# Kernel optimization log

Hardware: AMD Instinct MI355X
Metric: run time of the kernel (lower is better)

The kernel has to match this reference:

```python
import jax, jax.numpy as jnp
import numpy as np

N_NODES = 50000
N_EDGES = 400000
D_IN = 2048
D_OUT = 512


def setup_inputs() -> dict:
    key = jax.random.key(0)
    k1, k2, k3 = jax.random.split(key, 3)
    x = jax.random.normal(k1, (N_NODES, D_IN), dtype=jnp.float32)
    edge_index = jax.random.randint(k2, (2, N_EDGES), 0, N_NODES, dtype=jnp.int64)
    # Glorot init like PyG GCNConv
    scale = jnp.sqrt(6.0 / (D_IN + D_OUT)).astype(jnp.float32)
    weight = jax.random.uniform(k3, (D_IN, D_OUT), dtype=jnp.float32, minval=-scale, maxval=scale)
    bias = jnp.zeros((D_OUT,), dtype=jnp.float32)
    return {"x": x, "edge_index": edge_index, "weight": weight, "bias": bias}


def reference(x, edge_index, weight, bias):
    N = x.shape[0]
    # GCNConv(normalize=True): add self-loops, symmetric deg^-1/2 normalization
    loops = jnp.arange(N, dtype=edge_index.dtype)
    src = jnp.concatenate([edge_index[0], loops])  # message sources (x_j)
    dst = jnp.concatenate([edge_index[1], loops])  # aggregation targets
    ones = jnp.ones(dst.shape[0], dtype=x.dtype)
    deg = jax.ops.segment_sum(ones, dst, num_segments=N)  # [N]
    deg_inv_sqrt = jnp.where(deg > 0, jax.lax.rsqrt(deg), 0.0)
    norm = deg_inv_sqrt[src] * deg_inv_sqrt[dst]  # [E+N]
    h = x @ weight  # [N, d_out] linear transform before propagation
    msgs = norm[:, None] * h[src]  # [E+N, d_out]
    out = jax.ops.segment_sum(msgs, dst, num_segments=N) + bias  # [N, d_out]
    return jax.nn.log_softmax(out, axis=1)
```

## Files before the change

kernel.cpp:

```cpp
#include <hip/hip_runtime.h>
#include <stdint.h>

#define D_IN   2048
#define D_OUT  512

typedef __bf16 bf16;
typedef bf16     bf16x8 __attribute__((ext_vector_type(8)));
typedef float    f32x4  __attribute__((ext_vector_type(4)));
typedef uint32_t u32x4  __attribute__((ext_vector_type(4)));

#define GLP(p)  (const __attribute__((address_space(1))) void*)(p)
#define LDSP(p) (__attribute__((address_space(3))) void*)(p)

__global__ void k_count(const int* __restrict__ dstv, int* __restrict__ cnt, int E) {
    int e = blockIdx.x * blockDim.x + threadIdx.x;
    if (e < E) atomicAdd(&cnt[dstv[e]], 1);
}

__global__ __launch_bounds__(1024) void k_scan1(const int* __restrict__ cnt,
                                                int* __restrict__ offs,
                                                int* __restrict__ bsum,
                                                float* __restrict__ dis,
                                                int* __restrict__ cur, int n) {
    __shared__ int wsum[16], wbase[16];
    const int tid = threadIdx.x, lane = tid & 63, wv = tid >> 6;
    int i = blockIdx.x * 1024 + tid;
    int v = (i < n) ? cnt[i] : 0;
    int x = v;
    #pragma unroll
    for (int d = 1; d < 64; d <<= 1) {
        int y = __shfl_up(x, d);
        if (lane >= d) x += y;
    }
    if (lane == 63) wsum[wv] = x;
    __syncthreads();
    if (tid < 16) {
        int s = 0;
        for (int j = 0; j < tid; ++j) s += wsum[j];
        wbase[tid] = s;
    }
    __syncthreads();
    if (i < n) {
        offs[i] = wbase[wv] + x - v;
        dis[i]  = rsqrtf((float)(v + 1));
        cur[i]  = 0;
    }
    if (tid == 0) bsum[blockIdx.x] = wbase[15] + wsum[15];
}

__global__ void k_scan2(int* __restrict__ bsum, int nb) {
    int t = threadIdx.x;
    if (nb <= 64) {
        int v = (t < nb) ? bsum[t] : 0;
        int x = v;
        #pragma unroll
        for (int d = 1; d < 64; d <<= 1) {
            int y = __shfl_up(x, d);
            if (t >= d) x += y;
        }
        if (t < nb) bsum[t] = x - v;
    } else if (t == 0) {
        int run = 0;
        for (int j = 0; j < nb; ++j) { int v = bsum[j]; bsum[j] = run; run += v; }
    }
}

__global__ void k_fill(const int* __restrict__ srcv, const int* __restrict__ dstv,
                       const int* __restrict__ offs, const int* __restrict__ bsum,
                       const float* __restrict__ dis, int* __restrict__ cur,
                       int* __restrict__ csr, float* __restrict__ nrm, int E) {
    int e = blockIdx.x * blockDim.x + threadIdx.x;
    if (e < E) {
        int d = dstv[e];
        int s = srcv[e];
        int p = offs[d] + bsum[d >> 10] + atomicAdd(&cur[d], 1);
        csr[p] = s;
        nrm[p] = dis[s];
    }
}

__global__ void k_wt(const float* __restrict__ W, uint16_t* __restrict__ wt) {
    __shared__ float t[32][33];
    int kb = blockIdx.x * 32, nb = blockIdx.y * 32;
    int tx = threadIdx.x, ty = threadIdx.y;
    #pragma unroll
    for (int i = 0; i < 32; i += 8)
        t[ty + i][tx] = W[(size_t)(kb + ty + i) * D_OUT + nb + tx];
    __syncthreads();
    bf16* o = (bf16*)wt;
    #pragma unroll
    for (int i = 0; i < 32; i += 8)
        o[(size_t)(nb + ty + i) * D_IN + kb + tx] = (bf16)t[tx][ty + i];
}

__global__ __launch_bounds__(256, 3) void k_gemm(const float* __restrict__ X,
                                                 const uint16_t* __restrict__ WT,
                                                 uint16_t* __restrict__ H, int M) {
    __shared__ uint16_t lsA[128 * 64];
    __shared__ uint16_t lsB[2][128 * 64];
    const int nwg = gridDim.x;
    const int b = blockIdx.x;
    const int q = nwg >> 3, r = nwg & 7;
    const int xcd = b & 7, lo = b >> 3;
    const int g = (xcd < r) ? (xcd * (q + 1) + lo) : (r * (q + 1) + (xcd - r) * q + lo);
    const int m0 = (g >> 2) * 128;
    const int n0 = (g & 3) * 128;
    const int tid = threadIdx.x;
    const int w = tid >> 6, lane = tid & 63;
    const int wr = w >> 1, wc = w & 1;
    const int lr = lane & 15, lk = lane >> 4;
    const int NT = D_IN / 64;

    f32x4 acc[4][4];
    #pragma unroll
    for (int m = 0; m < 4; m++)
        #pragma unroll
        for (int n = 0; n < 4; n++) acc[m][n] = (f32x4)(0.0f);

    const float* aSrc[4];
    int aDst[4];
    const uint16_t* bSrc[4];
    #pragma unroll
    for (int j = 0; j < 4; j++) {
        int uidx = (w * 4 + j) * 64 + lane;
        int row = uidx >> 3, u = uidx & 7;
        int lrow = row;
        if (m0 + row >= M) lrow = (M - 1) - m0;
        aSrc[j] = X + (size_t)(m0 + lrow) * D_IN + u * 8;
        aDst[j] = row * 64 + (u ^ (row & 7)) * 8;
        bSrc[j] = WT + (size_t)(n0 + row) * D_IN + (u ^ (row & 7)) * 8;
    }

    f32x4 ar[8];

    auto loadA = [&](int t) {
        t &= (NT - 1);
        #pragma unroll
        for (int j = 0; j < 4; j++) {
            ar[2 * j]     = *(const f32x4*)(aSrc[j] + t * 64);
            ar[2 * j + 1] = *(const f32x4*)(aSrc[j] + t * 64 + 4);
        }
    };
    auto writeA = [&]() {
        #pragma unroll
        for (int j = 0; j < 4; j++) {
            f32x4 a0 = ar[2 * j], a1 = ar[2 * j + 1];
            bf16x8 tv;
            tv[0] = (bf16)a0[0]; tv[1] = (bf16)a0[1]; tv[2] = (bf16)a0[2]; tv[3] = (bf16)a0[3];
            tv[4] = (bf16)a1[0]; tv[5] = (bf16)a1[1]; tv[6] = (bf16)a1[2]; tv[7] = (bf16)a1[3];
            *(bf16x8*)(&lsA[aDst[j]]) = tv;
        }
    };
    auto stageB = [&](int t, int buf) {
        t &= (NT - 1);
        #pragma unroll
        for (int j = 0; j < 4; j++)
            __builtin_amdgcn_global_load_lds(GLP(bSrc[j] + t * 64),
                                             LDSP(&lsB[buf][(w * 4 + j) * 512]), 16, 0, 0);
    };
    auto compute = [&](int buf) {
        #pragma unroll
        for (int kk = 0; kk < 2; kk++) {
            bf16x8 aF[4], bF[4];
            #pragma unroll
            for (int m = 0; m < 4; m++) {
                int row = wr * 64 + m * 16 + lr;
                aF[m] = *(const bf16x8*)(&lsA[row * 64 + (((kk * 4 + lk) ^ (row & 7)) * 8)]);
            }
            #pragma unroll
            for (int n = 0; n < 4; n++) {
                int row = wc * 64 + n * 16 + lr;
                bF[n] = *(const bf16x8*)(&lsB[buf][row * 64 + (((kk * 4 + lk) ^ (row & 7)) * 8)]);
            }
            #pragma unroll
            for (int m = 0; m < 4; m++)
                #pragma unroll
                for (int n = 0; n < 4; n++)
                    acc[m][n] = __builtin_amdgcn_mfma_f32_16x16x32_bf16(aF[m], bF[n], acc[m][n], 0, 0, 0);
        }
    };

    loadA(0);
    stageB(0, 0);
    stageB(1, 1);
    asm volatile("s_waitcnt vmcnt(8)" ::: "memory");
    writeA();
    asm volatile("s_waitcnt vmcnt(4)" ::: "memory");
    asm volatile("s_waitcnt lgkmcnt(0)" ::: "memory");
    __builtin_amdgcn_s_barrier();

    #pragma unroll 1
    for (int t = 0; t < NT; t += 2) {
        loadA(t + 1);
        compute(0);
        __builtin_amdgcn_s_barrier();
        stageB(t + 2, 0);
        asm volatile("s_waitcnt vmcnt(4)" ::: "memory");
        writeA();
        asm volatile("s_waitcnt lgkmcnt(0)" ::: "memory");
        __builtin_amdgcn_s_barrier();
        loadA(t + 2);
        compute(1);
        __builtin_amdgcn_s_barrier();
        stageB(t + 3, 1);
        asm volatile("s_waitcnt vmcnt(4)" ::: "memory");
        writeA();
        asm volatile("s_waitcnt lgkmcnt(0)" ::: "memory");
        __builtin_amdgcn_s_barrier();
    }
    asm volatile("s_waitcnt vmcnt(0)" ::: "memory");

    #pragma unroll
    for (int m = 0; m < 4; m++) {
        int rbase = m0 + wr * 64 + m * 16 + lk * 4;
        #pragma unroll
        for (int n = 0; n < 4; n++) {
            int col = n0 + wc * 64 + n * 16 + lr;
            #pragma unroll
            for (int j = 0; j < 4; j++) {
                int row = rbase + j;
                if (row < M) {
                    bf16 tv = (bf16)acc[m][n][j];
                    H[(size_t)row * D_OUT + col] = __builtin_bit_cast(uint16_t, tv);
                }
            }
        }
    }
}

__global__ __launch_bounds__(256) void k_agg(const uint16_t* __restrict__ h,
                                             const int* __restrict__ csr,
                                             const float* __restrict__ nrm,
                                             const int* __restrict__ offs,
                                             const int* __restrict__ bsum,
                                             const int* __restrict__ cnt,
                                             const float* __restrict__ dis,
                                             const float* __restrict__ bias,
                                             float* __restrict__ out, int N) {
    const int wv = threadIdx.x >> 6, lane = threadIdx.x & 63;
    const int i = blockIdx.x * 4 + wv;
    if (i >= N) return;
    const float di = dis[i];
    float acc[8];
    {
        u32x4 v = *(const u32x4*)(h + (size_t)i * D_OUT + lane * 8);
        float s2 = di * di;
        #pragma unroll
        for (int k = 0; k < 4; k++) {
            acc[2 * k]     = __builtin_bit_cast(float, v[k] << 16) * s2;
            acc[2 * k + 1] = __builtin_bit_cast(float, v[k] & 0xffff0000u) * s2;
        }
    }
    const int o = offs[i] + bsum[i >> 10], cend = o + cnt[i];
    int e = o;
    for (; e + 4 <= cend; e += 4) {
        int s0 = csr[e], s1 = csr[e + 1], s2 = csr[e + 2], s3 = csr[e + 3];
        float w0 = di * nrm[e],     w1 = di * nrm[e + 1];
        float w2 = di * nrm[e + 2], w3 = di * nrm[e + 3];
        u32x4 v0 = *(const u32x4*)(h + (size_t)s0 * D_OUT + lane * 8);
        u32x4 v1 = *(const u32x4*)(h + (size_t)s1 * D_OUT + lane * 8);
        u32x4 v2 = *(const u32x4*)(h + (size_t)s2 * D_OUT + lane * 8);
        u32x4 v3 = *(const u32x4*)(h + (size_t)s3 * D_OUT + lane * 8);
        #pragma unroll
        for (int k = 0; k < 4; k++) {
            acc[2 * k]     += __builtin_bit_cast(float, v0[k] << 16) * w0
                            + __builtin_bit_cast(float, v1[k] << 16) * w1
                            + __builtin_bit_cast(float, v2[k] << 16) * w2
                            + __builtin_bit_cast(float, v3[k] << 16) * w3;
            acc[2 * k + 1] += __builtin_bit_cast(float, v0[k] & 0xffff0000u) * w0
                            + __builtin_bit_cast(float, v1[k] & 0xffff0000u) * w1
                            + __builtin_bit_cast(float, v2[k] & 0xffff0000u) * w2
                            + __builtin_bit_cast(float, v3[k] & 0xffff0000u) * w3;
        }
    }
    for (; e < cend; ++e) {
        int s0 = csr[e];
        float w0 = di * nrm[e];
        u32x4 v0 = *(const u32x4*)(h + (size_t)s0 * D_OUT + lane * 8);
        #pragma unroll
        for (int k = 0; k < 4; k++) {
            acc[2 * k]     += __builtin_bit_cast(float, v0[k] << 16) * w0;
            acc[2 * k + 1] += __builtin_bit_cast(float, v0[k] & 0xffff0000u) * w0;
        }
    }
    {
        const f32x4* bp = (const f32x4*)(bias + lane * 8);
        f32x4 b0 = bp[0], b1 = bp[1];
        #pragma unroll
        for (int k = 0; k < 4; k++) { acc[k] += b0[k]; acc[4 + k] += b1[k]; }
    }
    float mx = acc[0];
    #pragma unroll
    for (int k = 1; k < 8; k++) mx = fmaxf(mx, acc[k]);
    #pragma unroll
    for (int d = 1; d < 64; d <<= 1) mx = fmaxf(mx, __shfl_xor(mx, d));
    float se = 0.f;
    #pragma unroll
    for (int k = 0; k < 8; k++) se += expf(acc[k] - mx);
    #pragma unroll
    for (int d = 1; d < 64; d <<= 1) se += __shfl_xor(se, d);
    float lse = mx + logf(se);
    f32x4 o0, o1;
    #pragma unroll
    for (int k = 0; k < 4; k++) { o0[k] = acc[k] - lse; o1[k] = acc[4 + k] - lse; }
    f32x4* op = (f32x4*)(out + (size_t)i * D_OUT + lane * 8);
    op[0] = o0; op[1] = o1;
}

extern "C" void kernel_launch(void* const* d_in, const int* in_sizes, int n_in,
                              void* d_out, int out_size, void* d_ws, size_t ws_size,
                              hipStream_t stream) {
    const float* x    = (const float*)d_in[0];
    const int*   ei   = (const int*)d_in[1];
    const float* W    = (const float*)d_in[2];
    const float* bias = (const float*)d_in[3];
    float* out = (float*)d_out;

    const int N = in_sizes[0] / D_IN;
    const int E = in_sizes[1] / 2;
    const int* srcv = ei;
    const int* dstv = ei + E;

    char* p = (char*)d_ws;
    auto carve = [&](size_t b) { void* r = (void*)p; p += (b + 255) & ~(size_t)255; return r; };
    uint16_t* h    = (uint16_t*)carve((size_t)N * D_OUT * 2);
    uint16_t* wt   = (uint16_t*)carve((size_t)D_OUT * D_IN * 2);
    int*      cnt  = (int*)carve((size_t)N * 4);
    int*      cur  = (int*)carve((size_t)N * 4);
    float*    dis  = (float*)carve((size_t)N * 4);
    int*      offs = (int*)carve((size_t)N * 4);
    int*      csr  = (int*)carve((size_t)E * 4);
    float*    nrm  = (float*)carve((size_t)E * 4);
    int*      bsum = (int*)carve(1024 * 4);

    hipMemsetAsync(cnt, 0, (size_t)N * 4, stream);

    k_wt<<<dim3(D_IN / 32, D_OUT / 32), dim3(32, 8), 0, stream>>>(W, wt);
    k_count<<<(E + 255) / 256, 256, 0, stream>>>(dstv, cnt, E);
    const int nb = (N + 1023) / 1024;
    k_scan1<<<nb, 1024, 0, stream>>>(cnt, offs, bsum, dis, cur, N);
    k_scan2<<<1, 64, 0, stream>>>(bsum, nb);
    k_fill<<<(E + 255) / 256, 256, 0, stream>>>(srcv, dstv, offs, bsum, dis, cur, csr, nrm, E);

    k_gemm<<<((N + 127) / 128) * 4, 256, 0, stream>>>(x, wt, h, N);

    k_agg<<<(N + 3) / 4, 256, 0, stream>>>(h, csr, nrm, offs, bsum, cnt, dis, bias, out, N);
}
```

Measured before the change: 349.7 us.

## Restructure GEMM to 128x256 tiles with async fp32 A staging into LDS

The GEMM now uses 512-thread workgroups computing 128x256 output tiles, so each A tile is read from HBM half as often. A is staged as fp32 directly into LDS with global_load_lds, replacing the register round-trip, and is converted to bf16 when fragments are read. Loads for the next K-step are interleaved per m-row with MFMA work under barriers and setprio. This needs 128KB of dynamic LDS and gives one workgroup per CU, so there is less latency hiding from occupancy and more LDS traffic for the fp32 A reads.

```diff
diff --git a/kernel.cpp b/kernel.cpp
--- a/kernel.cpp
+++ b/kernel.cpp
@@ -93,21 +93,23 @@
         o[(size_t)(nb + ty + i) * D_IN + kb + tx] = (bf16)t[tx][ty + i];
 }
 
-__global__ __launch_bounds__(256, 3) void k_gemm(const float* __restrict__ X,
+__global__ __launch_bounds__(512, 1) void k_gemm(const float* __restrict__ X,
                                                  const uint16_t* __restrict__ WT,
                                                  uint16_t* __restrict__ H, int M) {
-    __shared__ uint16_t lsA[128 * 64];
-    __shared__ uint16_t lsB[2][128 * 64];
+    extern __shared__ char smem[];
+    float*    lsA = (float*)smem;
+    uint16_t* lsB = (uint16_t*)(smem + 65536);
+
     const int nwg = gridDim.x;
     const int b = blockIdx.x;
     const int q = nwg >> 3, r = nwg & 7;
     const int xcd = b & 7, lo = b >> 3;
     const int g = (xcd < r) ? (xcd * (q + 1) + lo) : (r * (q + 1) + (xcd - r) * q + lo);
-    const int m0 = (g >> 2) * 128;
-    const int n0 = (g & 3) * 128;
+    const int m0 = (g >> 1) * 128;
+    const int n0 = (g & 1) * 256;
     const int tid = threadIdx.x;
     const int w = tid >> 6, lane = tid & 63;
-    const int wr = w >> 1, wc = w & 1;
+    const int wr = w >> 2, wc = w & 3;
     const int lr = lane & 15, lk = lane >> 4;
     const int NT = D_IN / 64;
 
@@ -117,98 +119,104 @@
         #pragma unroll
         for (int n = 0; n < 4; n++) acc[m][n] = (f32x4)(0.0f);
 
-    const float* aSrc[4];
-    int aDst[4];
-    const uint16_t* bSrc[4];
-    #pragma unroll
-    for (int j = 0; j < 4; j++) {
-        int uidx = (w * 4 + j) * 64 + lane;
-        int row = uidx >> 3, u = uidx & 7;
-        int lrow = row;
-        if (m0 + row >= M) lrow = (M - 1) - m0;
-        aSrc[j] = X + (size_t)(m0 + lrow) * D_IN + u * 8;
-        aDst[j] = row * 64 + (u ^ (row & 7)) * 8;
-        bSrc[j] = WT + (size_t)(n0 + row) * D_IN + (u ^ (row & 7)) * 8;
-    }
-
-    f32x4 ar[8];
-
-    auto loadA = [&](int t) {
-        t &= (NT - 1);
-        #pragma unroll
-        for (int j = 0; j < 4; j++) {
-            ar[2 * j]     = *(const f32x4*)(aSrc[j] + t * 64);
-            ar[2 * j + 1] = *(const f32x4*)(aSrc[j] + t * 64 + 4);
+    const float* aS[4]; int aD[4];
+    #pragma unroll
+    for (int h = 0; h < 2; h++)
+        #pragma unroll
+        for (int j = 0; j < 2; j++) {
+            int L = h * 1024 + j * 512 + tid;
+            int row = L >> 4, u = L & 15;
+            int lrow = row;
+            if (m0 + row >= M) lrow = (M - 1) - m0;
+            aS[h * 2 + j] = X + (size_t)(m0 + lrow) * D_IN + (u ^ (row & 15)) * 4;
+            aD[h * 2 + j] = L * 4;
+        }
+    const uint16_t* bS[4]; int bD[4];
+    #pragma unroll
+    for (int h = 0; h < 2; h++)
+        #pragma unroll
+        for (int j = 0; j < 2; j++) {
+            int L = h * 1024 + j * 512 + tid;
+            int row = L >> 3, u = L & 7;
+            bS[h * 2 + j] = WT + (size_t)(n0 + row) * D_IN + (u ^ (row & 7)) * 8;
+            bD[h * 2 + j] = L * 8;
+        }
+
+    auto stageHalf = [&](int tn, int sn, int half) {
+        if (half < 2) {
+            #pragma unroll
+            for (int j = 0; j < 2; j++)
+                __builtin_amdgcn_global_load_lds(GLP(aS[half * 2 + j] + tn * 64),
+                    LDSP(lsA + sn * 8192 + aD[half * 2 + j]), 16, 0, 0);
+        } else {
+            #pragma unroll
+            for (int j = 0; j < 2; j++)
+                __builtin_amdgcn_global_load_lds(GLP(bS[(half - 2) * 2 + j] + tn * 64),
+                    LDSP(lsB + sn * 16384 + bD[(half - 2) * 2 + j]), 16, 0, 0);
         }
     };
-    auto writeA = [&]() {
-        #pragma unroll
-        for (int j = 0; j < 4; j++) {
-            f32x4 a0 = ar[2 * j], a1 = ar[2 * j + 1];
-            bf16x8 tv;
-            tv[0] = (bf16)a0[0]; tv[1] = (bf16)a0[1]; tv[2] = (bf16)a0[2]; tv[3] = (bf16)a0[3];
-            tv[4] = (bf16)a1[0]; tv[5] = (bf16)a1[1]; tv[6] = (bf16)a1[2]; tv[7] = (bf16)a1[3];
-            *(bf16x8*)(&lsA[aDst[j]]) = tv;
+
+    auto TILE = [&](int t, int sc, bool stageNext) {
+        const float*    A_c = lsA + sc * 8192;
+        const uint16_t* B_c = lsB + sc * 16384;
+        const int sn = sc ^ 1;
+        bf16x8 bF[4][2];
+        #pragma unroll
+        for (int m = 0; m < 4; m++) {
+            if (m == 0) {
+                #pragma unroll
+                for (int n = 0; n < 4; n++) {
+                    int row = wc * 64 + n * 16 + lr;
+                    #pragma unroll
+                    for (int kk = 0; kk < 2; kk++)
+                        bF[n][kk] = *(const bf16x8*)(B_c + row * 64 +
+                                     (((kk * 4 + lk) ^ (row & 7)) * 8));
+                }
+            }
+            bf16x8 aF[2];
+            {
+                int row = wr * 64 + m * 16 + lr;
+                const float* base = A_c + row * 64;
+                #pragma unroll
+                for (int kk = 0; kk < 2; kk++) {
+                    int u0 = kk * 8 + lk * 2;
+                    f32x4 a0 = *(const f32x4*)(base + ((u0    ) ^ (row & 15)) * 4);
+                    f32x4 a1 = *(const f32x4*)(base + ((u0 + 1) ^ (row & 15)) * 4);
+                    bf16x8 tv;
+                    tv[0] = (bf16)a0[0]; tv[1] = (bf16)a0[1]; tv[2] = (bf16)a0[2]; tv[3] = (bf16)a0[3];
+                    tv[4] = (bf16)a1[0]; tv[5] = (bf16)a1[1]; tv[6] = (bf16)a1[2]; tv[7] = (bf16)a1[3];
+                    aF[kk] = tv;
+                }
+            }
+            if (stageNext) stageHalf(t + 1, sn, m);
+            asm volatile("" ::: "memory");
+            __builtin_amdgcn_s_barrier();
+            asm volatile("" ::: "memory");
+            __builtin_amdgcn_s_setprio(1);
+            #pragma unroll
+            for (int n = 0; n < 4; n++)
+                #pragma unroll
+                for (int kk = 0; kk < 2; kk++)
+                    acc[m][n] = __builtin_amdgcn_mfma_f32_16x16x32_bf16(aF[kk], bF[n][kk], acc[m][n], 0, 0, 0);
+            __builtin_amdgcn_s_setprio(0);
+            if (m == 3)
+                asm volatile("s_waitcnt vmcnt(0)" ::: "memory");
+            asm volatile("" ::: "memory");
+            __builtin_amdgcn_s_barrier();
         }
     };
-    auto stageB = [&](int t, int buf) {
-        t &= (NT - 1);
-        #pragma unroll
-        for (int j = 0; j < 4; j++)
-            __builtin_amdgcn_global_load_lds(GLP(bSrc[j] + t * 64),
-                                             LDSP(&lsB[buf][(w * 4 + j) * 512]), 16, 0, 0);
-    };
-    auto compute = [&](int buf) {
-        #pragma unroll
-        for (int kk = 0; kk < 2; kk++) {
-            bf16x8 aF[4], bF[4];
-            #pragma unroll
-            for (int m = 0; m < 4; m++) {
-                int row = wr * 64 + m * 16 + lr;
-                aF[m] = *(const bf16x8*)(&lsA[row * 64 + (((kk * 4 + lk) ^ (row & 7)) * 8)]);
-            }
-            #pragma unroll
-            for (int n = 0; n < 4; n++) {
-                int row = wc * 64 + n * 16 + lr;
-                bF[n] = *(const bf16x8*)(&lsB[buf][row * 64 + (((kk * 4 + lk) ^ (row & 7)) * 8)]);
-            }
-            #pragma unroll
-            for (int m = 0; m < 4; m++)
-                #pragma unroll
-                for (int n = 0; n < 4; n++)
-                    acc[m][n] = __builtin_amdgcn_mfma_f32_16x16x32_bf16(aF[m], bF[n], acc[m][n], 0, 0, 0);
-        }
-    };
-
-    loadA(0);
-    stageB(0, 0);
-    stageB(1, 1);
-    asm volatile("s_waitcnt vmcnt(8)" ::: "memory");
-    writeA();
-    asm volatile("s_waitcnt vmcnt(4)" ::: "memory");
-    asm volatile("s_waitcnt lgkmcnt(0)" ::: "memory");
+
+    #pragma unroll
+    for (int hh = 0; hh < 4; hh++) stageHalf(0, 0, hh);
+    asm volatile("s_waitcnt vmcnt(0)" ::: "memory");
     __builtin_amdgcn_s_barrier();
+    asm volatile("" ::: "memory");
 
     #pragma unroll 1
     for (int t = 0; t < NT; t += 2) {
-        loadA(t + 1);
-        compute(0);
-        __builtin_amdgcn_s_barrier();
-        stageB(t + 2, 0);
-        asm volatile("s_waitcnt vmcnt(4)" ::: "memory");
-        writeA();
-        asm volatile("s_waitcnt lgkmcnt(0)" ::: "memory");
-        __builtin_amdgcn_s_barrier();
-        loadA(t + 2);
-        compute(1);
-        __builtin_amdgcn_s_barrier();
-        stageB(t + 3, 1);
-        asm volatile("s_waitcnt vmcnt(4)" ::: "memory");
-        writeA();
-        asm volatile("s_waitcnt lgkmcnt(0)" ::: "memory");
-        __builtin_amdgcn_s_barrier();
-    }
-    asm volatile("s_waitcnt vmcnt(0)" ::: "memory");
+        TILE(t,     0, true);
+        TILE(t + 1, 1, t + 2 < NT);
+    }
 
     #pragma unroll
     for (int m = 0; m < 4; m++) {
@@ -335,6 +343,9 @@
 
     hipMemsetAsync(cnt, 0, (size_t)N * 4, stream);
 
+    hipFuncSetAttribute((const void*)k_gemm,
+                        hipFuncAttributeMaxDynamicSharedMemorySize, 131072);
+
     k_wt<<<dim3(D_IN / 32, D_OUT / 32), dim3(32, 8), 0, stream>>>(W, wt);
     k_count<<<(E + 255) / 256, 256, 0, stream>>>(dstv, cnt, E);
     const int nb = (N + 1023) / 1024;
@@ -342,7 +353,8 @@
     k_scan2<<<1, 64, 0, stream>>>(bsum, nb);
     k_fill<<<(E + 255) / 256, 256, 0, stream>>>(srcv, dstv, offs, bsum, dis, cur, csr, nrm, E);
 
-    k_gemm<<<((N + 127) / 128) * 4, 256, 0, stream>>>(x, wt, h, N);
+    const int nmB = (N + 127) / 128;
+    k_gemm<<<nmB * 2, 512, 131072, stream>>>(x, wt, h, N);
 
     k_agg<<<(N + 3) / 4, 256, 0, stream>>>(h, csr, nrm, offs, bsum, cnt, dis, bias, out, N);
 }
```

After: 344.7 us. Within noise of the previous version (-1.4%).

## Double-buffer A register prefetch in GEMM and unroll aggregation by two

Applied to the files above, without the earlier changes.

The GEMM main loop now keeps two register sets for A tiles, so A loads are issued two stages ahead and the vmcnt waits are relaxed to allow more loads in flight. The aim is to hide global-load latency behind MFMA compute, at the cost of eight more f32x4 registers per thread, which may lower occupancy. Separately, the gather-aggregate loop is unrolled by two instead of four, with sequential accumulation. That shortens the tail handling and lowers register pressure but leaves fewer gather loads in flight at once.

```diff
diff --git a/kernel.cpp b/kernel.cpp
--- a/kernel.cpp
+++ b/kernel.cpp
@@ -131,20 +131,20 @@
         bSrc[j] = WT + (size_t)(n0 + row) * D_IN + (u ^ (row & 7)) * 8;
     }
 
-    f32x4 ar[8];
-
-    auto loadA = [&](int t) {
+    f32x4 setA[8], setB[8];
+
+    auto loadA = [&](f32x4* s, int t) {
         t &= (NT - 1);
         #pragma unroll
         for (int j = 0; j < 4; j++) {
-            ar[2 * j]     = *(const f32x4*)(aSrc[j] + t * 64);
-            ar[2 * j + 1] = *(const f32x4*)(aSrc[j] + t * 64 + 4);
+            s[2 * j]     = *(const f32x4*)(aSrc[j] + t * 64);
+            s[2 * j + 1] = *(const f32x4*)(aSrc[j] + t * 64 + 4);
         }
     };
-    auto writeA = [&]() {
+    auto writeA = [&](const f32x4* s) {
         #pragma unroll
         for (int j = 0; j < 4; j++) {
-            f32x4 a0 = ar[2 * j], a1 = ar[2 * j + 1];
+            f32x4 a0 = s[2 * j], a1 = s[2 * j + 1];
             bf16x8 tv;
             tv[0] = (bf16)a0[0]; tv[1] = (bf16)a0[1]; tv[2] = (bf16)a0[2]; tv[3] = (bf16)a0[3];
             tv[4] = (bf16)a1[0]; tv[5] = (bf16)a1[1]; tv[6] = (bf16)a1[2]; tv[7] = (bf16)a1[3];
@@ -180,31 +180,31 @@
         }
     };
 
-    loadA(0);
+    loadA(setA, 0);
     stageB(0, 0);
+    asm volatile("s_waitcnt vmcnt(0)" ::: "memory");
+    writeA(setA);
     stageB(1, 1);
-    asm volatile("s_waitcnt vmcnt(8)" ::: "memory");
-    writeA();
-    asm volatile("s_waitcnt vmcnt(4)" ::: "memory");
+    loadA(setB, 1);
     asm volatile("s_waitcnt lgkmcnt(0)" ::: "memory");
     __builtin_amdgcn_s_barrier();
 
     #pragma unroll 1
     for (int t = 0; t < NT; t += 2) {
-        loadA(t + 1);
+        loadA(setA, t + 2);
         compute(0);
         __builtin_amdgcn_s_barrier();
         stageB(t + 2, 0);
-        asm volatile("s_waitcnt vmcnt(4)" ::: "memory");
-        writeA();
+        asm volatile("s_waitcnt vmcnt(12)" ::: "memory");
+        writeA(setB);
         asm volatile("s_waitcnt lgkmcnt(0)" ::: "memory");
         __builtin_amdgcn_s_barrier();
-        loadA(t + 2);
+        loadA(setB, t + 3);
         compute(1);
         __builtin_amdgcn_s_barrier();
         stageB(t + 3, 1);
-        asm volatile("s_waitcnt vmcnt(4)" ::: "memory");
-        writeA();
+        asm volatile("s_waitcnt vmcnt(12)" ::: "memory");
+        writeA(setA);
         asm volatile("s_waitcnt lgkmcnt(0)" ::: "memory");
         __builtin_amdgcn_s_barrier();
     }
@@ -251,29 +251,25 @@
             acc[2 * k + 1] = __builtin_bit_cast(float, v[k] & 0xffff0000u) * s2;
         }
     }
-    const int o = offs[i] + bsum[i >> 10], cend = o + cnt[i];
+    const int o = offs[i] + bsum[i >> 10], c = cnt[i];
     int e = o;
-    for (; e + 4 <= cend; e += 4) {
-        int s0 = csr[e], s1 = csr[e + 1], s2 = csr[e + 2], s3 = csr[e + 3];
-        float w0 = di * nrm[e],     w1 = di * nrm[e + 1];
-        float w2 = di * nrm[e + 2], w3 = di * nrm[e + 3];
+    for (; e + 2 <= o + c; e += 2) {
+        int s0 = csr[e], s1 = csr[e + 1];
+        float w0 = di * nrm[e], w1 = di * nrm[e + 1];
         u32x4 v0 = *(const u32x4*)(h + (size_t)s0 * D_OUT + lane * 8);
         u32x4 v1 = *(const u32x4*)(h + (size_t)s1 * D_OUT + lane * 8);
-        u32x4 v2 = *(const u32x4*)(h + (size_t)s2 * D_OUT + lane * 8);
-        u32x4 v3 = *(const u32x4*)(h + (size_t)s3 * D_OUT + lane * 8);
         #pragma unroll
         for (int k = 0; k < 4; k++) {
-            acc[2 * k]     += __builtin_bit_cast(float, v0[k] << 16) * w0
-                            + __builtin_bit_cast(float, v1[k] << 16) * w1
-                            + __builtin_bit_cast(float, v2[k] << 16) * w2
-                            + __builtin_bit_cast(float, v3[k] << 16) * w3;
-            acc[2 * k + 1] += __builtin_bit_cast(float, v0[k] & 0xffff0000u) * w0
-                            + __builtin_bit_cast(float, v1[k] & 0xffff0000u) * w1
-                            + __builtin_bit_cast(float, v2[k] & 0xffff0000u) * w2
-                            + __builtin_bit_cast(float, v3[k] & 0xffff0000u) * w3;
-        }
-    }
-    for (; e < cend; ++e) {
+            acc[2 * k]     += __builtin_bit_cast(float, v0[k] << 16) * w0;
+            acc[2 * k + 1] += __builtin_bit_cast(float, v0[k] & 0xffff0000u) * w0;
+        }
+        #pragma unroll
+        for (int k = 0; k < 4; k++) {
+            acc[2 * k]     += __builtin_bit_cast(float, v1[k] << 16) * w1;
+            acc[2 * k + 1] += __builtin_bit_cast(float, v1[k] & 0xffff0000u) * w1;
+        }
+    }
+    if (e < o + c) {
         int s0 = csr[e];
         float w0 = di * nrm[e];
         u32x4 v0 = *(const u32x4*)(h + (size_t)s0 * D_OUT + lane * 8);
```

New measurement: 387.3 us. 10.7% more time.
